# Kernel optimization log

Hardware: AMD Instinct MI355X
Metric: run time of the kernel (lower is better)

Reference implementation:

```python
import jax, jax.numpy as jnp
import numpy as np

N, D_IN, D_H, K, E = 100000, 128, 256, 16, 3200000


def setup_inputs() -> dict:
    key = jax.random.key(0)
    ks = jax.random.split(key, 6)
    x = jax.random.normal(ks[0], (N, D_IN), dtype=jnp.float32)
    edge_index = jax.random.randint(ks[1], (2, E), 0, N, dtype=jnp.int64)
    # Linear params (stored as [in, out] for x @ W + b)
    W1 = jax.random.normal(ks[2], (D_IN, D_H), dtype=jnp.float32) * 0.05
    b1 = jnp.zeros((D_H,), dtype=jnp.float32)
    W2 = jax.random.normal(ks[3], (D_H, K), dtype=jnp.float32) * 0.05
    b2 = jnp.zeros((K,), dtype=jnp.float32)
    return {"x": x, "edge_index": edge_index, "W1": W1, "b1": b1, "W2": W2, "b2": b2}


def reference(x, edge_index, W1, b1, W2, b2):
    # 2-layer MLP + row softmax -> soft cluster assignments C [N, K]
    h = jax.nn.relu(x @ W1 + b1)
    C = jax.nn.softmax(h @ W2 + b2, axis=1)
    # trace((C C^T)^T @ adj) == sum over edges (u,v) of C[u] . C[v]
    # (exact, incl. duplicate edges, since to_dense_adj scatter-adds 1 per edge)
    src, dst = edge_index[0], edge_index[1]
    edge_sum = jnp.sum(C[src] * C[dst])  # [E, K] gathered dot products, reduced
    num_edges = jnp.asarray(edge_index.shape[1], dtype=C.dtype)  # adj.sum()
    modularity_loss = -edge_sum / num_edges
    return (C, modularity_loss)
```

## Files before the change

### kernel.cpp

```cpp
#include <hip/hip_runtime.h>

#define N_NODES 100000
#define D_INF   128
#define D_HID   256
#define K_CL    16
#define N_EDGES 3200000
#define N_TILES (N_NODES / 16)

typedef __attribute__((ext_vector_type(8))) __bf16  bf16x8;
typedef __attribute__((ext_vector_type(8))) unsigned short u16x8;
typedef __attribute__((ext_vector_type(4))) float   f32x4;

__device__ __forceinline__ unsigned short f2bf(float f) {
    unsigned int u = __builtin_bit_cast(unsigned int, f);
    u += 0x7fffu + ((u >> 16) & 1u);
    return (unsigned short)(u >> 16);
}
__device__ __forceinline__ float bflo(unsigned int p) {
    return __builtin_bit_cast(float, p << 16);
}
__device__ __forceinline__ float bfhi(unsigned int p) {
    return __builtin_bit_cast(float, p & 0xffff0000u);
}

__global__ void prep_kernel(const float* __restrict__ W1,
                            const float* __restrict__ W2,
                            unsigned short* __restrict__ w1t,
                            unsigned short* __restrict__ w2t,
                            float* __restrict__ acc)
{
    const int i = blockIdx.x * 256 + threadIdx.x;
    if (i == 0) *acc = 0.f;
    if (i < D_INF * D_HID) {
        const int n = i >> 7, k = i & 127;
        w1t[i] = f2bf(W1[k * D_HID + n]);
    }
    if (i < D_HID * K_CL) {
        const int t = i >> 8, n = i & 255;
        w2t[i] = f2bf(W2[n * K_CL + t]);
    }
}

#define W1S 136
#define CHS 40

__global__ __launch_bounds__(256, 2) void mlp_kernel(
    const float* __restrict__ x, const unsigned short* __restrict__ W1T,
    const float* __restrict__ b1, const unsigned short* __restrict__ W2T,
    const float* __restrict__ b2, float* __restrict__ C,
    unsigned short* __restrict__ Cb)
{
    __shared__ unsigned short w1s[256 * W1S];
    __shared__ unsigned short chbuf[4][2][16 * CHS];
    __shared__ float b1s[D_HID];

    const int tid  = threadIdx.x;
    const int wv   = tid >> 6;
    const int lane = tid & 63;
    const int c    = lane & 15;
    const int q    = lane >> 4;

    #pragma unroll
    for (int it = 0; it < 16; ++it) {
        const int idx = it * 256 + tid;
        const int row = idx >> 4, ch = idx & 15;
        const uint4 v = ((const uint4*)W1T)[idx];
        *(uint4*)&w1s[row * W1S + ch * 8] = v;
    }
    if (tid < D_HID) b1s[tid] = b1[tid];

    bf16x8 w2f[8];
    #pragma unroll
    for (int kc2 = 0; kc2 < 8; ++kc2)
        w2f[kc2] = *(const bf16x8*)(W2T + (size_t)c * D_HID + kc2 * 32 + q * 8);
    const float b2v = b2[c];
    __syncthreads();

    unsigned short* const chA = &chbuf[wv][0][0];
    unsigned short* const chB = &chbuf[wv][1][0];

    const int wid     = blockIdx.x * 4 + wv;
    const int wstride = gridDim.x * 4;

    for (int tile = wid; tile < N_TILES; tile += wstride) {
        const int m0 = tile * 16;

        const float* xrow = x + (size_t)(m0 + c) * D_INF + q * 8;
        bf16x8 afr[4];
        #pragma unroll
        for (int kc = 0; kc < 4; ++kc) {
            const float4 xa = *(const float4*)(xrow + kc * 32);
            const float4 xb = *(const float4*)(xrow + kc * 32 + 4);
            u16x8 af;
            af[0] = f2bf(xa.x); af[1] = f2bf(xa.y); af[2] = f2bf(xa.z); af[3] = f2bf(xa.w);
            af[4] = f2bf(xb.x); af[5] = f2bf(xb.y); af[6] = f2bf(xb.z); af[7] = f2bf(xb.w);
            afr[kc] = __builtin_bit_cast(bf16x8, af);
        }

        f32x4 acc2 = (f32x4){0.f, 0.f, 0.f, 0.f};
        #pragma unroll
        for (int kc2 = 0; kc2 < 8; ++kc2) {
            unsigned short* const cb = (kc2 & 1) ? chB : chA;
            #pragma unroll
            for (int half = 0; half < 2; ++half) {
                const int nt = kc2 * 2 + half;
                f32x4 a1 = (f32x4){0.f, 0.f, 0.f, 0.f};
                #pragma unroll
                for (int kc = 0; kc < 4; ++kc) {
                    const bf16x8 bf =
                        *(const bf16x8*)&w1s[(nt * 16 + c) * W1S + kc * 32 + q * 8];
                    a1 = __builtin_amdgcn_mfma_f32_16x16x32_bf16(afr[kc], bf, a1, 0, 0, 0);
                }
                const float bv = b1s[nt * 16 + c];
                #pragma unroll
                for (int r = 0; r < 4; ++r)
                    cb[(4 * q + r) * CHS + half * 16 + c] =
                        f2bf(fmaxf(a1[r] + bv, 0.f));
            }
            const bf16x8 a2 = *(const bf16x8*)&cb[c * CHS + q * 8];
            acc2 = __builtin_amdgcn_mfma_f32_16x16x32_bf16(a2, w2f[kc2], acc2, 0, 0, 0);
        }

        #pragma unroll
        for (int r = 0; r < 4; ++r) {
            const float l = acc2[r] + b2v;
            float mx = l;
            mx = fmaxf(mx, __shfl_xor(mx, 1));
            mx = fmaxf(mx, __shfl_xor(mx, 2));
            mx = fmaxf(mx, __shfl_xor(mx, 4));
            mx = fmaxf(mx, __shfl_xor(mx, 8));
            const float e = __expf(l - mx);
            float sm = e;
            sm += __shfl_xor(sm, 1);
            sm += __shfl_xor(sm, 2);
            sm += __shfl_xor(sm, 4);
            sm += __shfl_xor(sm, 8);
            const float p = e / sm;
            const size_t o = (size_t)(m0 + 4 * q + r) * K_CL + c;
            C[o]  = p;
            Cb[o] = f2bf(p);
        }
    }
}

__global__ __launch_bounds__(256) void edge_kernel(
    const int* __restrict__ ei, const unsigned short* __restrict__ Cb,
    float* __restrict__ acc)
{
    __shared__ float red[4];
    const int tid  = threadIdx.x;
    const int lane = tid & 63;
    const int wv   = tid >> 6;
    const int t    = lane & 3;
    const int g    = lane >> 2;

    const long long wid    = (long long)blockIdx.x * 4 + wv;
    const long long stride = (long long)gridDim.x * 4 * 32;

    float s = 0.f;
    for (long long base = wid * 32; base < N_EDGES; base += stride) {
        const long long e0 = base + g, e1 = e0 + 16;
        const int u0 = ei[e0], v0 = ei[N_EDGES + e0];
        const int u1 = ei[e1], v1 = ei[N_EDGES + e1];
        const uint2 a0 = *(const uint2*)(Cb + (size_t)u0 * K_CL + t * 4);
        const uint2 b0 = *(const uint2*)(Cb + (size_t)v0 * K_CL + t * 4);
        const uint2 a1 = *(const uint2*)(Cb + (size_t)u1 * K_CL + t * 4);
        const uint2 b1 = *(const uint2*)(Cb + (size_t)v1 * K_CL + t * 4);
        s = fmaf(bflo(a0.x), bflo(b0.x), s);
        s = fmaf(bfhi(a0.x), bfhi(b0.x), s);
        s = fmaf(bflo(a0.y), bflo(b0.y), s);
        s = fmaf(bfhi(a0.y), bfhi(b0.y), s);
        s = fmaf(bflo(a1.x), bflo(b1.x), s);
        s = fmaf(bfhi(a1.x), bfhi(b1.x), s);
        s = fmaf(bflo(a1.y), bflo(b1.y), s);
        s = fmaf(bfhi(a1.y), bfhi(b1.y), s);
    }
    s += __shfl_xor(s, 1);
    s += __shfl_xor(s, 2);
    s += __shfl_xor(s, 4);
    s += __shfl_xor(s, 8);
    s += __shfl_xor(s, 16);
    s += __shfl_xor(s, 32);
    if (lane == 0) red[wv] = s;
    __syncthreads();
    if (tid == 0) atomicAdd(acc, red[0] + red[1] + red[2] + red[3]);
}

__global__ void finalize_kernel(const float* __restrict__ acc,
                                float* __restrict__ out)
{
    out[(size_t)N_NODES * K_CL] = -acc[0] / (float)N_EDGES;
}

extern "C" void kernel_launch(void* const* d_in, const int* in_sizes, int n_in,
                              void* d_out, int out_size, void* d_ws, size_t ws_size,
                              hipStream_t stream) {
    const float* x  = (const float*)d_in[0];
    const int*   ei = (const int*)  d_in[1];
    const float* W1 = (const float*)d_in[2];
    const float* b1 = (const float*)d_in[3];
    const float* W2 = (const float*)d_in[4];
    const float* b2 = (const float*)d_in[5];
    float* out = (float*)d_out;

    unsigned short* w1t = (unsigned short*)d_ws;
    unsigned short* w2t = (unsigned short*)((char*)d_ws + 65536);
    float*          acc = (float*)((char*)d_ws + 73728);
    unsigned short* Cb  = (unsigned short*)((char*)d_ws + 73760);

    prep_kernel<<<128, 256, 0, stream>>>(W1, W2, w1t, w2t, acc);
    mlp_kernel<<<512, 256, 0, stream>>>(x, w1t, b1, w2t, b2, out, Cb);
    edge_kernel<<<1024, 256, 0, stream>>>(ei, Cb, acc);
    finalize_kernel<<<1, 1, 0, stream>>>(acc, out);
}
```

Baseline: 161.1 us.

## Restructure edge kernel with coalesced index loads, 16-byte gathers, block partials

The edge kernel is rewritten as one-shot blocks that each handle 512 edges. Each wave loads its 128 src and 128 dst indices with coalesced per-lane loads and distributes them to lanes with shuffles. Each edge's row is then gathered by two lanes with 16-byte loads instead of four lanes with 8-byte loads. The global atomic accumulator is replaced by per-block partial sums that a 256-thread finalize kernel reduces, which removes the accumulator zeroing in prep. The cost is a much larger grid (6250 blocks) and an extra partials buffer in the workspace.

Result: faster. 155.2 us (-3.7%).

```diff
diff --git a/kernel.cpp b/kernel.cpp
--- a/kernel.cpp
+++ b/kernel.cpp
@@ -6,6 +6,7 @@
 #define K_CL    16
 #define N_EDGES 3200000
 #define N_TILES (N_NODES / 16)
+#define EDGE_BLOCKS (N_EDGES / 512)
 
 typedef __attribute__((ext_vector_type(8))) __bf16  bf16x8;
 typedef __attribute__((ext_vector_type(8))) unsigned short u16x8;
@@ -26,11 +27,9 @@
 __global__ void prep_kernel(const float* __restrict__ W1,
                             const float* __restrict__ W2,
                             unsigned short* __restrict__ w1t,
-                            unsigned short* __restrict__ w2t,
-                            float* __restrict__ acc)
+                            unsigned short* __restrict__ w2t)
 {
     const int i = blockIdx.x * 256 + threadIdx.x;
-    if (i == 0) *acc = 0.f;
     if (i < D_INF * D_HID) {
         const int n = i >> 7, k = i & 127;
         w1t[i] = f2bf(W1[k * D_HID + n]);
@@ -145,35 +144,38 @@
 
 __global__ __launch_bounds__(256) void edge_kernel(
     const int* __restrict__ ei, const unsigned short* __restrict__ Cb,
-    float* __restrict__ acc)
+    float* __restrict__ partials)
 {
     __shared__ float red[4];
     const int tid  = threadIdx.x;
     const int lane = tid & 63;
     const int wv   = tid >> 6;
-    const int t    = lane & 3;
-    const int g    = lane >> 2;
-
-    const long long wid    = (long long)blockIdx.x * 4 + wv;
-    const long long stride = (long long)gridDim.x * 4 * 32;
+    const int base = (blockIdx.x * 4 + wv) * 128;
+
+    const int u0 = ei[base + lane];
+    const int u1 = ei[base + 64 + lane];
+    const int v0 = ei[N_EDGES + base + lane];
+    const int v1 = ei[N_EDGES + base + 64 + lane];
+
+    const int half8 = (lane & 1) * 8;
+    const int sl    = lane >> 1;
 
     float s = 0.f;
-    for (long long base = wid * 32; base < N_EDGES; base += stride) {
-        const long long e0 = base + g, e1 = e0 + 16;
-        const int u0 = ei[e0], v0 = ei[N_EDGES + e0];
-        const int u1 = ei[e1], v1 = ei[N_EDGES + e1];
-        const uint2 a0 = *(const uint2*)(Cb + (size_t)u0 * K_CL + t * 4);
-        const uint2 b0 = *(const uint2*)(Cb + (size_t)v0 * K_CL + t * 4);
-        const uint2 a1 = *(const uint2*)(Cb + (size_t)u1 * K_CL + t * 4);
-        const uint2 b1 = *(const uint2*)(Cb + (size_t)v1 * K_CL + t * 4);
-        s = fmaf(bflo(a0.x), bflo(b0.x), s);
-        s = fmaf(bfhi(a0.x), bfhi(b0.x), s);
-        s = fmaf(bflo(a0.y), bflo(b0.y), s);
-        s = fmaf(bfhi(a0.y), bfhi(b0.y), s);
-        s = fmaf(bflo(a1.x), bflo(b1.x), s);
-        s = fmaf(bfhi(a1.x), bfhi(b1.x), s);
-        s = fmaf(bflo(a1.y), bflo(b1.y), s);
-        s = fmaf(bfhi(a1.y), bfhi(b1.y), s);
+    #pragma unroll
+    for (int g = 0; g < 4; ++g) {
+        const int src = (g & 1) * 32 + sl;
+        const int ue  = __shfl((g < 2) ? u0 : u1, src);
+        const int ve  = __shfl((g < 2) ? v0 : v1, src);
+        const uint4 a = *(const uint4*)(Cb + (size_t)ue * K_CL + half8);
+        const uint4 b = *(const uint4*)(Cb + (size_t)ve * K_CL + half8);
+        s = fmaf(bflo(a.x), bflo(b.x), s);
+        s = fmaf(bfhi(a.x), bfhi(b.x), s);
+        s = fmaf(bflo(a.y), bflo(b.y), s);
+        s = fmaf(bfhi(a.y), bfhi(b.y), s);
+        s = fmaf(bflo(a.z), bflo(b.z), s);
+        s = fmaf(bfhi(a.z), bfhi(b.z), s);
+        s = fmaf(bflo(a.w), bflo(b.w), s);
+        s = fmaf(bfhi(a.w), bfhi(b.w), s);
     }
     s += __shfl_xor(s, 1);
     s += __shfl_xor(s, 2);
@@ -183,13 +185,27 @@
     s += __shfl_xor(s, 32);
     if (lane == 0) red[wv] = s;
     __syncthreads();
-    if (tid == 0) atomicAdd(acc, red[0] + red[1] + red[2] + red[3]);
-}
-
-__global__ void finalize_kernel(const float* __restrict__ acc,
-                                float* __restrict__ out)
-{
-    out[(size_t)N_NODES * K_CL] = -acc[0] / (float)N_EDGES;
+    if (tid == 0) partials[blockIdx.x] = red[0] + red[1] + red[2] + red[3];
+}
+
+__global__ __launch_bounds__(256) void finalize_kernel(
+    const float* __restrict__ partials, float* __restrict__ out)
+{
+    __shared__ float red[4];
+    const int tid = threadIdx.x;
+    float s = 0.f;
+    for (int i = tid; i < EDGE_BLOCKS; i += 256) s += partials[i];
+    s += __shfl_xor(s, 1);
+    s += __shfl_xor(s, 2);
+    s += __shfl_xor(s, 4);
+    s += __shfl_xor(s, 8);
+    s += __shfl_xor(s, 16);
+    s += __shfl_xor(s, 32);
+    if ((tid & 63) == 0) red[tid >> 6] = s;
+    __syncthreads();
+    if (tid == 0)
+        out[(size_t)N_NODES * K_CL] =
+            -(red[0] + red[1] + red[2] + red[3]) / (float)N_EDGES;
 }
 
 extern "C" void kernel_launch(void* const* d_in, const int* in_sizes, int n_in,
@@ -203,13 +219,13 @@
     const float* b2 = (const float*)d_in[5];
     float* out = (float*)d_out;
 
-    unsigned short* w1t = (unsigned short*)d_ws;
-    unsigned short* w2t = (unsigned short*)((char*)d_ws + 65536);
-    float*          acc = (float*)((char*)d_ws + 73728);
-    unsigned short* Cb  = (unsigned short*)((char*)d_ws + 73760);
-
-    prep_kernel<<<128, 256, 0, stream>>>(W1, W2, w1t, w2t, acc);
+    unsigned short* w1t      = (unsigned short*)d_ws;
+    unsigned short* w2t      = (unsigned short*)((char*)d_ws + 65536);
+    unsigned short* Cb       = (unsigned short*)((char*)d_ws + 73760);
+    float*          partials = (float*)((char*)d_ws + 3273760);
+
+    prep_kernel<<<128, 256, 0, stream>>>(W1, W2, w1t, w2t);
     mlp_kernel<<<512, 256, 0, stream>>>(x, w1t, b1, w2t, b2, out, Cb);
-    edge_kernel<<<1024, 256, 0, stream>>>(ei, Cb, acc);
-    finalize_kernel<<<1, 1, 0, stream>>>(acc, out);
-}
+    edge_kernel<<<EDGE_BLOCKS, 256, 0, stream>>>(ei, Cb, partials);
+    finalize_kernel<<<1, 256, 0, stream>>>(partials, out);
+}
```
